# Kernel optimization log

Measured on AMD Instinct MI355X. Metric: run time of the kernel, lower is better.

The kernel has to match this reference:

```python
import jax, jax.numpy as jnp
import numpy as np

N = 100000
E = 1600000
H = 128
L = 3


def setup_inputs() -> dict:
    key = jax.random.key(0)
    ks = jax.random.split(key, 8)
    z = jax.random.normal(ks[0], (N, H), dtype=jnp.float32)
    edge_index = jax.random.randint(ks[1], (2, E), 0, N, dtype=jnp.int64)
    edge_weight = jax.random.uniform(ks[2], (E,), dtype=jnp.float32)
    s = 1.0 / np.sqrt(H)
    weight = jax.random.uniform(ks[3], (L, H, H), minval=-s, maxval=s, dtype=jnp.float32)
    w_ih = jax.random.uniform(ks[4], (3 * H, H), minval=-s, maxval=s, dtype=jnp.float32)
    w_hh = jax.random.uniform(ks[5], (3 * H, H), minval=-s, maxval=s, dtype=jnp.float32)
    b_ih = jax.random.uniform(ks[6], (3 * H,), minval=-s, maxval=s, dtype=jnp.float32)
    b_hh = jax.random.uniform(ks[7], (3 * H,), minval=-s, maxval=s, dtype=jnp.float32)
    return {"z": z, "edge_weight": edge_weight, "weight": weight,
            "w_ih": w_ih, "w_hh": w_hh, "b_ih": b_ih, "b_hh": b_hh,
            "edge_index": edge_index}


def _gru_cell(m, h, w_ih, w_hh, b_ih, b_hh):
    # torch GRUCell: gate order (r, z, n)
    gi = m @ w_ih.T + b_ih   # [N, 3H]
    gh = h @ w_hh.T + b_hh   # [N, 3H]
    i_r, i_z, i_n = jnp.split(gi, 3, axis=-1)
    h_r, h_z, h_n = jnp.split(gh, 3, axis=-1)
    r = jax.nn.sigmoid(i_r + h_r)
    zg = jax.nn.sigmoid(i_z + h_z)
    n = jnp.tanh(i_n + r * h_n)
    return (1.0 - zg) * n + zg * h


def reference(z, edge_weight, weight, w_ih, w_hh, b_ih, b_hh, edge_index):
    src = edge_index[0]  # x_j gathered from source nodes
    dst = edge_index[1]  # aggregated at target nodes
    x = z  # in_channels == out_channels, so no zero padding needed
    for l in range(L):
        m = x @ weight[l]                                  # [N, H]
        msg = m[src] * edge_weight[:, None]                # [E, H]
        agg = jax.ops.segment_sum(msg, dst, num_segments=N)  # aggr='add'
        x = _gru_cell(agg, x, w_ih, w_hh, b_ih, b_hh)
    return x
```

## Files before the change

kernel.cpp:

```cpp
#include <hip/hip_runtime.h>

typedef __bf16 bf16x8 __attribute__((ext_vector_type(8)));
typedef float floatx4 __attribute__((ext_vector_type(4)));

#define NPB 256
#define NPB_SHIFT 8
#define MAXNB 1024
#define TILE 4096

static __device__ __forceinline__ float bfu_to_f(unsigned short u) {
    unsigned int x = ((unsigned int)u) << 16;
    return __builtin_bit_cast(float, x);
}
static __device__ __forceinline__ unsigned short f_to_bfu(float f) {
    unsigned int u = __builtin_bit_cast(unsigned int, f);
    unsigned int r = (u + 0x7fffu + ((u >> 16) & 1u)) >> 16;
    return (unsigned short)r;
}

__global__ void detect_k(const unsigned short* __restrict__ bih_u,
                         const unsigned int* __restrict__ ei_u,
                         int* __restrict__ flags) {
    __shared__ int sv, sz;
    int t = threadIdx.x;
    if (t == 0) { sv = 0; sz = 0; }
    __syncthreads();
    unsigned short u = bih_u[2 * t];
    unsigned int ex = (u >> 7) & 0xFF;
    if (ex >= 64 && ex < 124) atomicAdd(&sv, 1);
    if (ei_u[2 * t + 1] == 0u) atomicAdd(&sz, 1);
    __syncthreads();
    if (t == 0) {
        flags[0] = (sv >= 48) ? 1 : 0;
        flags[1] = (sz == 64) ? 1 : 0;
    }
}


__global__ void cvt_bf16_k(const void* __restrict__ in, unsigned short* __restrict__ out,
                           int n, const int* __restrict__ flags) {
    int i = blockIdx.x * 256 + threadIdx.x;
    if (i >= n) return;
    if (flags[0]) out[i] = ((const unsigned short*)in)[i];
    else out[i] = f_to_bfu(((const float*)in)[i]);
}

__global__ void cvt_bias_k(const void* __restrict__ bih, const void* __restrict__ bhh,
                           float* __restrict__ bih_f, float* __restrict__ bhh_f,
                           const int* __restrict__ flags) {
    int i = blockIdx.x * 256 + threadIdx.x;
    if (i >= 768) return;
    const void* src = (i < 384) ? bih : bhh;
    int j = (i < 384) ? i : i - 384;
    float v = flags[0] ? bfu_to_f(((const unsigned short*)src)[j]) : ((const float*)src)[j];
    if (i < 384) bih_f[j] = v;
    else bhh_f[j] = v;
}

__global__ void out_k(const unsigned short* __restrict__ xb, void* __restrict__ out,
                      int n, const int* __restrict__ flags) {
    int i = blockIdx.x * 256 + threadIdx.x;
    if (i >= n) return;
    if (flags[0]) ((unsigned short*)out)[i] = xb[i];
    else ((float*)out)[i] = bfu_to_f(xb[i]);
}


static __device__ __forceinline__ int load_idx(const unsigned int* eiu, size_t pos, int is64) {
    return (int)eiu[is64 ? 2 * pos : pos];
}

__global__ __launch_bounds__(256) void count_k(const unsigned int* __restrict__ eiu,
                                               int* __restrict__ bucketCnt, int E,
                                               const int* __restrict__ flags) {
    __shared__ int cnt[MAXNB];
    int t = threadIdx.x;
    for (int b = t; b < MAXNB; b += 256) cnt[b] = 0;
    __syncthreads();
    int is64 = flags[1];
    int e0 = blockIdx.x * TILE;
    int e1 = min(e0 + TILE, E);
    for (int e = e0 + t; e < e1; e += 256) {
        int d = load_idx(eiu, (size_t)E + e, is64);
        atomicAdd(&cnt[d >> NPB_SHIFT], 1);
    }
    __syncthreads();
    for (int b = t; b < MAXNB; b += 256) {
        int c = cnt[b];
        if (c) atomicAdd(&bucketCnt[b], c);
    }
}

__global__ void scanB_k(const int* __restrict__ bucketCnt, int* __restrict__ bucketBase,
                        int* __restrict__ bucketCursor, int NB, int E) {
    __shared__ int sh[MAXNB];
    int t = threadIdx.x;
    int v = (t < NB) ? bucketCnt[t] : 0;
    sh[t] = v;
    __syncthreads();
    for (int off = 1; off < MAXNB; off <<= 1) {
        int u = (t >= off) ? sh[t - off] : 0;
        __syncthreads();
        sh[t] += u;
        __syncthreads();
    }
    if (t < NB) {
        int b = sh[t] - v;
        bucketBase[t] = b;
        bucketCursor[t] = b;
    }
    if (t == 0) bucketBase[NB] = E;
}

__global__ __launch_bounds__(256) void bin_k(const unsigned int* __restrict__ eiu,
                                             const void* __restrict__ ew,
                                             int* __restrict__ bucketCursor,
                                             uint2* __restrict__ rec8, int E,
                                             const int* __restrict__ flags) {
    __shared__ int cnt[MAXNB];
    __shared__ int basel[MAXNB];
    int t = threadIdx.x;
    for (int b = t; b < MAXNB; b += 256) cnt[b] = 0;
    __syncthreads();
    int is64 = flags[1];
    int isb = flags[0];
    int e0 = blockIdx.x * TILE;
    int e1 = min(e0 + TILE, E);
    for (int e = e0 + t; e < e1; e += 256) {
        int d = load_idx(eiu, (size_t)E + e, is64);
        atomicAdd(&cnt[d >> NPB_SHIFT], 1);
    }
    __syncthreads();
    for (int b = t; b < MAXNB; b += 256) {
        int c = cnt[b];
        basel[b] = c ? atomicAdd(&bucketCursor[b], c) : 0;
        cnt[b] = 0;
    }
    __syncthreads();
    for (int e = e0 + t; e < e1; e += 256) {
        int s = load_idx(eiu, (size_t)e, is64);
        int d = load_idx(eiu, (size_t)E + e, is64);
        float w = isb ? bfu_to_f(((const unsigned short*)ew)[e]) : ((const float*)ew)[e];
        int b = d >> NPB_SHIFT;
        int p = basel[b] + atomicAdd(&cnt[b], 1);
        rec8[p] = make_uint2((unsigned int)s | ((unsigned int)(d & 255) << 20),
                             __builtin_bit_cast(unsigned int, w));
    }
}

__global__ __launch_bounds__(256) void csr_k(const uint2* __restrict__ rec8,
                                             const int* __restrict__ bucketBase,
                                             int* __restrict__ offsets,
                                             uint2* __restrict__ rec, int N, int E) {
    __shared__ int cnt[NPB];
    __shared__ int sh[NPB];
    __shared__ int cur[NPB];
    int t = threadIdx.x;
    int b = blockIdx.x;
    int n0 = b << NPB_SHIFT;
    int nodes = min(NPB, N - n0);
    int ebase = bucketBase[b];
    int ecnt = bucketBase[b + 1] - ebase;

    cnt[t] = 0;
    __syncthreads();
    for (int i = t; i < ecnt; i += 256) {
        int d = (rec8[ebase + i].x >> 20) & 255;
        atomicAdd(&cnt[d], 1);
    }
    __syncthreads();
    int v = cnt[t];
    sh[t] = v;
    __syncthreads();
    for (int off = 1; off < NPB; off <<= 1) {
        int u = (t >= off) ? sh[t - off] : 0;
        __syncthreads();
        sh[t] += u;
        __syncthreads();
    }
    int loff = sh[t] - v;
    if (t < nodes) offsets[n0 + t] = ebase + loff;
    cur[t] = ebase + loff;
    if (b == 0 && t == 0) offsets[N] = E;
    __syncthreads();
    for (int i = t; i < ecnt; i += 256) {
        uint2 r = rec8[ebase + i];
        int d = (r.x >> 20) & 255;
        int p = atomicAdd(&cur[d], 1);
        rec[p] = make_uint2(r.x & 0xFFFFFu, r.y);
    }
}


static __device__ __forceinline__ float dot8_bf(uint4 wv, uint4 iv) {
    float s;
    s  = bfu_to_f((unsigned short)(wv.x)) * bfu_to_f((unsigned short)(iv.x));
    s += bfu_to_f((unsigned short)(wv.x >> 16)) * bfu_to_f((unsigned short)(iv.x >> 16));
    s += bfu_to_f((unsigned short)(wv.y)) * bfu_to_f((unsigned short)(iv.y));
    s += bfu_to_f((unsigned short)(wv.y >> 16)) * bfu_to_f((unsigned short)(iv.y >> 16));
    s += bfu_to_f((unsigned short)(wv.z)) * bfu_to_f((unsigned short)(iv.z));
    s += bfu_to_f((unsigned short)(wv.z >> 16)) * bfu_to_f((unsigned short)(iv.z >> 16));
    s += bfu_to_f((unsigned short)(wv.w)) * bfu_to_f((unsigned short)(iv.w));
    s += bfu_to_f((unsigned short)(wv.w >> 16)) * bfu_to_f((unsigned short)(iv.w >> 16));
    return s;
}

__global__ void make_ut_k(const void* __restrict__ weight, const void* __restrict__ wih,
                          unsigned short* __restrict__ Ut, const int* __restrict__ flags) {
    int idx = blockIdx.x * 256 + threadIdx.x;
    if (idx >= 3 * 384 * 128) return;
    int isb = flags[0];
    int a = idx & 127;
    int j = (idx >> 7) % 384;
    int l = idx / (384 * 128);
    float s = 0.f;
    if (isb) {
        const uint4* W4 = (const uint4*)((const unsigned short*)weight + (size_t)l * 16384 + a * 128);
        const uint4* I4 = (const uint4*)((const unsigned short*)wih + (size_t)j * 128);
#pragma unroll
        for (int c = 0; c < 16; c++) s += dot8_bf(W4[c], I4[c]);
    } else {
        const float4* W4 = (const float4*)((const float*)weight + (size_t)l * 16384 + a * 128);
        const float4* I4 = (const float4*)((const float*)wih + (size_t)j * 128);
#pragma unroll
        for (int c = 0; c < 32; c++) {
            float4 w = W4[c], i = I4[c];
            s += w.x * i.x + w.y * i.y + w.z * i.z + w.w * i.w;
        }
    }
    Ut[idx] = f_to_bfu(s);
}

__global__ void pack_b_k(const unsigned short* __restrict__ Ut,
                         const void* __restrict__ whh,
                         unsigned short* __restrict__ Bp,
                         const int* __restrict__ flags) {
    int idx = blockIdx.x * 256 + threadIdx.x;
    if (idx >= 3 * 4 * 12 * 4 * 64) return;
    int lane = idx & 63;
    int kc = (idx >> 6) & 3;
    int rest = idx >> 8;
    int j = rest % 12;
    int cg = (rest / 12) & 3;
    int l = rest / 48;
    int s = j / 6;
    int g = (j % 6) >> 1;
    int t = j & 1;
    int col = (cg * 2 + t) * 16 + (lane & 15);
    int k = kc * 32 + (lane >> 4) * 8;
    int row384 = g * 128 + col;
    unsigned short tmp[8];
    const unsigned short* src;
    if (s == 0) {
        src = Ut + (size_t)l * 49152 + row384 * 128 + k;
    } else if (flags[0]) {
        src = (const unsigned short*)whh + (size_t)row384 * 128 + k;
    } else {
        const float* wf = (const float*)whh + (size_t)row384 * 128 + k;
        for (int i = 0; i < 8; i++) tmp[i] = f_to_bfu(wf[i]);
        src = tmp;
    }
    unsigned short* dst = Bp + (size_t)l * 98304 + (((size_t)(cg * 12 + j) * 4 + kc) * 64 + lane) * 8;
    for (int i = 0; i < 8; i++) dst[i] = src[i];
}


__global__ __launch_bounds__(256) void agg_k(const unsigned short* __restrict__ xb,
                                             const int* __restrict__ offs,
                                             const uint2* __restrict__ rec,
                                             unsigned short* __restrict__ y, int N,
                                             int nch) {
    int bid = blockIdx.x;
    int c = ((bid & 7) << 3) + ((bid >> 3) & 7) + ((bid >> 6) << 6);
    if (c >= nch) return;
    int node = c * 16 + (threadIdx.x >> 4);
    int l16 = threadIdx.x & 15;
    if (node >= N) return;
    int b = offs[node];
    int e2 = offs[node + 1];
    const uint4* xp4 = (const uint4*)xb;
    float a0[8], a1[8];
#pragma unroll
    for (int i = 0; i < 8; i++) { a0[i] = 0.f; a1[i] = 0.f; }

    auto fma_row = [&](float* acc, uint4 v, float w) {
        acc[0] += w * __builtin_bit_cast(float, v.x << 16);
        acc[1] += w * __builtin_bit_cast(float, v.x & 0xffff0000u);
        acc[2] += w * __builtin_bit_cast(float, v.y << 16);
        acc[3] += w * __builtin_bit_cast(float, v.y & 0xffff0000u);
        acc[4] += w * __builtin_bit_cast(float, v.z << 16);
        acc[5] += w * __builtin_bit_cast(float, v.z & 0xffff0000u);
        acc[6] += w * __builtin_bit_cast(float, v.w << 16);
        acc[7] += w * __builtin_bit_cast(float, v.w & 0xffff0000u);
    };

    int e = b;
    for (; e + 4 <= e2; e += 4) {
        uint2 r0 = rec[e], r1 = rec[e + 1], r2 = rec[e + 2], r3 = rec[e + 3];
        uint4 v0 = xp4[(size_t)r0.x * 16 + l16];
        uint4 v1 = xp4[(size_t)r1.x * 16 + l16];
        uint4 v2 = xp4[(size_t)r2.x * 16 + l16];
        uint4 v3 = xp4[(size_t)r3.x * 16 + l16];
        fma_row(a0, v0, __builtin_bit_cast(float, r0.y));
        fma_row(a1, v1, __builtin_bit_cast(float, r1.y));
        fma_row(a0, v2, __builtin_bit_cast(float, r2.y));
        fma_row(a1, v3, __builtin_bit_cast(float, r3.y));
    }
    for (; e < e2; e++) {
        uint2 r = rec[e];
        uint4 v = xp4[(size_t)r.x * 16 + l16];
        fma_row(a0, v, __builtin_bit_cast(float, r.y));
    }

    uint4 o;
    o.x = (unsigned int)f_to_bfu(a0[0] + a1[0]) | ((unsigned int)f_to_bfu(a0[1] + a1[1]) << 16);
    o.y = (unsigned int)f_to_bfu(a0[2] + a1[2]) | ((unsigned int)f_to_bfu(a0[3] + a1[3]) << 16);
    o.z = (unsigned int)f_to_bfu(a0[4] + a1[4]) | ((unsigned int)f_to_bfu(a0[5] + a1[5]) << 16);
    o.w = (unsigned int)f_to_bfu(a0[6] + a1[6]) | ((unsigned int)f_to_bfu(a0[7] + a1[7]) << 16);
    ((uint4*)y)[(size_t)node * 16 + l16] = o;
}


__global__ __launch_bounds__(512, 4) void gru_k(const unsigned short* __restrict__ y,
                                                const unsigned short* __restrict__ xin,
                                                unsigned short* __restrict__ xout,
                                                const unsigned short* __restrict__ Bp,
                                                const float* __restrict__ bih,
                                                const float* __restrict__ bhh, int N) {
    __shared__ uint4 Blds[3072];

    int bid = blockIdx.x;
    int r8 = bid & 7;
    int inner = bid >> 3;
    int cg = inner & 3;
    int rb = ((inner >> 2) << 3) + r8;
    int row0 = rb << 7;
    if (row0 >= N) return;

    int tid = threadIdx.x;
    {
        const uint4* bsrc = (const uint4*)(Bp + (size_t)cg * 24576);
#pragma unroll
        for (int i = 0; i < 6; i++) Blds[tid + i * 512] = bsrc[tid + i * 512];
    }
    __syncthreads();

    int wave = tid >> 6;
    int wc = wave & 1;
    int wr = wave >> 1;
    int lane = tid & 63;
    int quad = lane >> 4;
    int m16 = lane & 15;
    const unsigned short* bl = (const unsigned short*)Blds;

    int rA[2];
#pragma unroll
    for (int rt = 0; rt < 2; rt++) {
        int r = row0 + wr * 32 + rt * 16 + m16;
        rA[rt] = (r < N) ? r : N - 1;
    }

    floatx4 acc[2][4];
#pragma unroll
    for (int rt = 0; rt < 2; rt++)
#pragma unroll
        for (int s = 0; s < 4; s++) acc[rt][s] = (floatx4){0.f, 0.f, 0.f, 0.f};

    bf16x8 aY[2][4], aX[2][4];

#pragma unroll
    for (int rt = 0; rt < 2; rt++)
#pragma unroll
        for (int kc = 0; kc < 4; kc++)
            aY[rt][kc] = *(const bf16x8*)(y + (size_t)rA[rt] * 128 + kc * 32 + quad * 8);
    __builtin_amdgcn_sched_barrier(0);

#pragma unroll
    for (int rt = 0; rt < 2; rt++)
#pragma unroll
        for (int kc = 0; kc < 4; kc++)
            aX[rt][kc] = *(const bf16x8*)(xin + (size_t)rA[rt] * 128 + kc * 32 + quad * 8);

#pragma unroll
    for (int kc = 0; kc < 4; kc++) {
#pragma unroll
        for (int g = 0; g < 3; g++) {
            int jU = g * 2 + wc;
            bf16x8 b = *(const bf16x8*)(bl + ((size_t)(jU * 4 + kc) * 64 + lane) * 8);
            int s = (g == 2) ? 2 : g;
            acc[0][s] = __builtin_amdgcn_mfma_f32_16x16x32_bf16(aY[0][kc], b, acc[0][s], 0, 0, 0);
            acc[1][s] = __builtin_amdgcn_mfma_f32_16x16x32_bf16(aY[1][kc], b, acc[1][s], 0, 0, 0);
        }
    }
    __builtin_amdgcn_sched_barrier(0);

#pragma unroll
    for (int kc = 0; kc < 4; kc++) {
#pragma unroll
        for (int g = 0; g < 3; g++) {
            int jW = 6 + g * 2 + wc;
            bf16x8 b = *(const bf16x8*)(bl + ((size_t)(jW * 4 + kc) * 64 + lane) * 8);
            int s = (g == 2) ? 3 : g;
            acc[0][s] = __builtin_amdgcn_mfma_f32_16x16x32_bf16(aX[0][kc], b, acc[0][s], 0, 0, 0);
            acc[1][s] = __builtin_amdgcn_mfma_f32_16x16x32_bf16(aX[1][kc], b, acc[1][s], 0, 0, 0);
        }
    }

    int ch = cg * 32 + wc * 16 + m16;
    float b_r = bih[ch] + bhh[ch];
    float b_z = bih[128 + ch] + bhh[128 + ch];
    float bi_n = bih[256 + ch];
    float bh_n = bhh[256 + ch];
#pragma unroll
    for (int rt = 0; rt < 2; rt++) {
#pragma unroll
        for (int ri = 0; ri < 4; ri++) {
            int row = row0 + wr * 32 + rt * 16 + quad * 4 + ri;
            if (row >= N) continue;
            float sr = acc[rt][0][ri] + b_r;
            float sz = acc[rt][1][ri] + b_z;
            float gn = acc[rt][2][ri] + bi_n;
            float hn = acc[rt][3][ri] + bh_n;
            float r = __builtin_amdgcn_rcpf(1.f + __expf(-sr));
            float zg = __builtin_amdgcn_rcpf(1.f + __expf(-sz));
            float x2 = gn + r * hn;
            float n = 1.f - 2.f * __builtin_amdgcn_rcpf(1.f + __expf(2.f * x2));
            float h = bfu_to_f(xin[(size_t)row * 128 + ch]);
            float o = n + zg * (h - n);
            xout[(size_t)row * 128 + ch] = f_to_bfu(o);
        }
    }
}


extern "C" void kernel_launch(void* const* d_in, const int* in_sizes, int n_in,
                              void* d_out, int out_size, void* d_ws, size_t ws_size,
                              hipStream_t stream) {
    const int N = in_sizes[0] / 128;
    const int E = in_sizes[1];
    const int NB = (N + NPB - 1) >> NPB_SHIFT;

    const void* z = d_in[0];
    const void* ew = d_in[1];
    const void* weight = d_in[2];
    const void* wih = d_in[3];
    const void* whh = d_in[4];
    const void* bih = d_in[5];
    const void* bhh = d_in[6];
    const unsigned int* eiu = (const unsigned int*)d_in[7];

    unsigned short* y = (unsigned short*)d_out;

    size_t off = 0;
    char* base = (char*)d_ws;
    auto carve = [&](size_t bytes) -> void* {
        void* p = base + off;
        off = (off + bytes + 255) & ~(size_t)255;
        return p;
    };
    unsigned short* xb = (unsigned short*)carve((size_t)N * 128 * 2);
    unsigned short* xb2 = (unsigned short*)carve((size_t)N * 128 * 2);
    uint2* rec8 = (uint2*)carve((size_t)E * 8);
    uint2* rec = (uint2*)carve((size_t)E * 8);
    int* offsets = (int*)carve((size_t)(N + 1) * 4);
    int* bucketCnt = (int*)carve(MAXNB * 4);
    int* bucketBase = (int*)carve((MAXNB + 1) * 4);
    int* bucketCursor = (int*)carve(MAXNB * 4);
    unsigned short* Ut = (unsigned short*)carve((size_t)3 * 384 * 128 * 2);
    unsigned short* Bp = (unsigned short*)carve((size_t)3 * 48 * 4 * 64 * 8 * 2);
    float* bih_f = (float*)carve(384 * 4);
    float* bhh_f = (float*)carve(384 * 4);
    int* flags = (int*)carve(256);

    detect_k<<<1, 64, 0, stream>>>((const unsigned short*)bih, eiu, flags);

    cvt_bf16_k<<<(N * 128 + 255) / 256, 256, 0, stream>>>(z, xb, N * 128, flags);
    cvt_bias_k<<<3, 256, 0, stream>>>(bih, bhh, bih_f, bhh_f, flags);

    hipMemsetAsync(bucketCnt, 0, MAXNB * 4, stream);
    int gbin = (E + TILE - 1) / TILE;
    count_k<<<gbin, 256, 0, stream>>>(eiu, bucketCnt, E, flags);
    scanB_k<<<1, MAXNB, 0, stream>>>(bucketCnt, bucketBase, bucketCursor, NB, E);
    bin_k<<<gbin, 256, 0, stream>>>(eiu, ew, bucketCursor, rec8, E, flags);
    csr_k<<<NB, NPB, 0, stream>>>(rec8, bucketBase, offsets, rec, N, E);

    make_ut_k<<<(3 * 384 * 128 + 255) / 256, 256, 0, stream>>>(weight, wih, Ut, flags);
    pack_b_k<<<(3 * 4 * 12 * 4 * 64 + 255) / 256, 256, 0, stream>>>(Ut, whh, Bp, flags);

    const int RB = (N + 127) >> 7;
    const int grid_gru = 8 * ((RB + 7) >> 3) * 4;
    const int nch = (N + 15) >> 4;
    const int grid_agg = ((nch + 63) >> 6) << 6;

    const unsigned short* cur = xb;
    unsigned short* nxt = xb2;
    for (int l = 0; l < 3; l++) {
        agg_k<<<grid_agg, 256, 0, stream>>>(cur, offsets, rec, y, N, nch);
        gru_k<<<grid_gru, 512, 0, stream>>>(y, cur, nxt, Bp + (size_t)l * 98304,
                                            bih_f, bhh_f, N);
        const unsigned short* tmp = cur;
        cur = nxt;
        nxt = (unsigned short*)tmp;
    }

    out_k<<<(N * 128 + 255) / 256, 256, 0, stream>>>(cur, d_out, N * 128, flags);
}
```

Before: 607.4 us.

## Fuse neighbor aggregation into GRU kernel via LDS-staged aggregated rows

Merges the gather-aggregate kernel and the GRU MFMA kernel into one kernel per layer. Each block aggregates its 128 rows into a swizzled LDS buffer, then loops over the four output column groups, prefetching the next weight slice into registers. This removes the global write and re-read of the aggregated activations and one launch per layer. In exchange it lowers block count and occupancy for the latency-bound gather, and serialises the column groups with extra barriers.

```diff
diff --git a/kernel.cpp b/kernel.cpp
--- a/kernel.cpp
+++ b/kernel.cpp
@@ -265,84 +265,78 @@
 }
 
 
-__global__ __launch_bounds__(256) void agg_k(const unsigned short* __restrict__ xb,
-                                             const int* __restrict__ offs,
-                                             const uint2* __restrict__ rec,
-                                             unsigned short* __restrict__ y, int N,
-                                             int nch) {
-    int bid = blockIdx.x;
-    int c = ((bid & 7) << 3) + ((bid >> 3) & 7) + ((bid >> 6) << 6);
-    if (c >= nch) return;
-    int node = c * 16 + (threadIdx.x >> 4);
-    int l16 = threadIdx.x & 15;
-    if (node >= N) return;
-    int b = offs[node];
-    int e2 = offs[node + 1];
-    const uint4* xp4 = (const uint4*)xb;
-    float a0[8], a1[8];
-#pragma unroll
-    for (int i = 0; i < 8; i++) { a0[i] = 0.f; a1[i] = 0.f; }
-
-    auto fma_row = [&](float* acc, uint4 v, float w) {
-        acc[0] += w * __builtin_bit_cast(float, v.x << 16);
-        acc[1] += w * __builtin_bit_cast(float, v.x & 0xffff0000u);
-        acc[2] += w * __builtin_bit_cast(float, v.y << 16);
-        acc[3] += w * __builtin_bit_cast(float, v.y & 0xffff0000u);
-        acc[4] += w * __builtin_bit_cast(float, v.z << 16);
-        acc[5] += w * __builtin_bit_cast(float, v.z & 0xffff0000u);
-        acc[6] += w * __builtin_bit_cast(float, v.w << 16);
-        acc[7] += w * __builtin_bit_cast(float, v.w & 0xffff0000u);
-    };
-
-    int e = b;
-    for (; e + 4 <= e2; e += 4) {
-        uint2 r0 = rec[e], r1 = rec[e + 1], r2 = rec[e + 2], r3 = rec[e + 3];
-        uint4 v0 = xp4[(size_t)r0.x * 16 + l16];
-        uint4 v1 = xp4[(size_t)r1.x * 16 + l16];
-        uint4 v2 = xp4[(size_t)r2.x * 16 + l16];
-        uint4 v3 = xp4[(size_t)r3.x * 16 + l16];
-        fma_row(a0, v0, __builtin_bit_cast(float, r0.y));
-        fma_row(a1, v1, __builtin_bit_cast(float, r1.y));
-        fma_row(a0, v2, __builtin_bit_cast(float, r2.y));
-        fma_row(a1, v3, __builtin_bit_cast(float, r3.y));
-    }
-    for (; e < e2; e++) {
-        uint2 r = rec[e];
-        uint4 v = xp4[(size_t)r.x * 16 + l16];
-        fma_row(a0, v, __builtin_bit_cast(float, r.y));
-    }
-
-    uint4 o;
-    o.x = (unsigned int)f_to_bfu(a0[0] + a1[0]) | ((unsigned int)f_to_bfu(a0[1] + a1[1]) << 16);
-    o.y = (unsigned int)f_to_bfu(a0[2] + a1[2]) | ((unsigned int)f_to_bfu(a0[3] + a1[3]) << 16);
-    o.z = (unsigned int)f_to_bfu(a0[4] + a1[4]) | ((unsigned int)f_to_bfu(a0[5] + a1[5]) << 16);
-    o.w = (unsigned int)f_to_bfu(a0[6] + a1[6]) | ((unsigned int)f_to_bfu(a0[7] + a1[7]) << 16);
-    ((uint4*)y)[(size_t)node * 16 + l16] = o;
-}
-
-
-__global__ __launch_bounds__(512, 4) void gru_k(const unsigned short* __restrict__ y,
-                                                const unsigned short* __restrict__ xin,
-                                                unsigned short* __restrict__ xout,
-                                                const unsigned short* __restrict__ Bp,
-                                                const float* __restrict__ bih,
-                                                const float* __restrict__ bhh, int N) {
+__global__ __launch_bounds__(512, 4) void fused_k(const unsigned short* __restrict__ xin,
+                                                  unsigned short* __restrict__ xout,
+                                                  const int* __restrict__ offs,
+                                                  const uint2* __restrict__ rec,
+                                                  const unsigned short* __restrict__ Bp,
+                                                  const float* __restrict__ bih,
+                                                  const float* __restrict__ bhh, int N) {
+    __shared__ unsigned short Ylds[16384];
     __shared__ uint4 Blds[3072];
 
-    int bid = blockIdx.x;
-    int r8 = bid & 7;
-    int inner = bid >> 3;
-    int cg = inner & 3;
-    int rb = ((inner >> 2) << 3) + r8;
-    int row0 = rb << 7;
-    if (row0 >= N) return;
-
     int tid = threadIdx.x;
+    int row0 = blockIdx.x << 7;
+
+    uint4 breg[6];
     {
-        const uint4* bsrc = (const uint4*)(Bp + (size_t)cg * 24576);
-#pragma unroll
-        for (int i = 0; i < 6; i++) Blds[tid + i * 512] = bsrc[tid + i * 512];
-    }
+        const uint4* bsrc = (const uint4*)Bp;
+#pragma unroll
+        for (int i = 0; i < 6; i++) breg[i] = bsrc[tid + i * 512];
+    }
+
+    {
+        const uint4* xp4 = (const uint4*)xin;
+        int l16 = tid & 15;
+        int rr = tid >> 4;
+        auto fma_row = [&](float* acc, uint4 v, float w) {
+            acc[0] += w * __builtin_bit_cast(float, v.x << 16);
+            acc[1] += w * __builtin_bit_cast(float, v.x & 0xffff0000u);
+            acc[2] += w * __builtin_bit_cast(float, v.y << 16);
+            acc[3] += w * __builtin_bit_cast(float, v.y & 0xffff0000u);
+            acc[4] += w * __builtin_bit_cast(float, v.z << 16);
+            acc[5] += w * __builtin_bit_cast(float, v.z & 0xffff0000u);
+            acc[6] += w * __builtin_bit_cast(float, v.w << 16);
+            acc[7] += w * __builtin_bit_cast(float, v.w & 0xffff0000u);
+        };
+        for (int gi = 0; gi < 4; gi++) {
+            int r = gi * 32 + rr;
+            int node = row0 + r;
+            float a0[8], a1[8];
+#pragma unroll
+            for (int i = 0; i < 8; i++) { a0[i] = 0.f; a1[i] = 0.f; }
+            if (node < N) {
+                int e = offs[node];
+                int e2 = offs[node + 1];
+                for (; e + 4 <= e2; e += 4) {
+                    uint2 r0 = rec[e], r1 = rec[e + 1], r2 = rec[e + 2], r3 = rec[e + 3];
+                    uint4 v0 = xp4[(size_t)r0.x * 16 + l16];
+                    uint4 v1 = xp4[(size_t)r1.x * 16 + l16];
+                    uint4 v2 = xp4[(size_t)r2.x * 16 + l16];
+                    uint4 v3 = xp4[(size_t)r3.x * 16 + l16];
+                    fma_row(a0, v0, __builtin_bit_cast(float, r0.y));
+                    fma_row(a1, v1, __builtin_bit_cast(float, r1.y));
+                    fma_row(a0, v2, __builtin_bit_cast(float, r2.y));
+                    fma_row(a1, v3, __builtin_bit_cast(float, r3.y));
+                }
+                for (; e < e2; e++) {
+                    uint2 rr2 = rec[e];
+                    uint4 v = xp4[(size_t)rr2.x * 16 + l16];
+                    fma_row(a0, v, __builtin_bit_cast(float, rr2.y));
+                }
+            }
+            uint4 o;
+            o.x = (unsigned int)f_to_bfu(a0[0] + a1[0]) | ((unsigned int)f_to_bfu(a0[1] + a1[1]) << 16);
+            o.y = (unsigned int)f_to_bfu(a0[2] + a1[2]) | ((unsigned int)f_to_bfu(a0[3] + a1[3]) << 16);
+            o.z = (unsigned int)f_to_bfu(a0[4] + a1[4]) | ((unsigned int)f_to_bfu(a0[5] + a1[5]) << 16);
+            o.w = (unsigned int)f_to_bfu(a0[6] + a1[6]) | ((unsigned int)f_to_bfu(a0[7] + a1[7]) << 16);
+            int u = l16 ^ (r & 15);
+            *(uint4*)&Ylds[(size_t)r * 128 + u * 8] = o;
+        }
+    }
+
+#pragma unroll
+    for (int i = 0; i < 6; i++) Blds[tid + i * 512] = breg[i];
     __syncthreads();
 
     int wave = tid >> 6;
@@ -353,81 +347,90 @@
     int m16 = lane & 15;
     const unsigned short* bl = (const unsigned short*)Blds;
 
-    int rA[2];
+    int rloc[2], rA[2];
 #pragma unroll
     for (int rt = 0; rt < 2; rt++) {
-        int r = row0 + wr * 32 + rt * 16 + m16;
-        rA[rt] = (r < N) ? r : N - 1;
-    }
-
-    floatx4 acc[2][4];
-#pragma unroll
-    for (int rt = 0; rt < 2; rt++)
-#pragma unroll
-        for (int s = 0; s < 4; s++) acc[rt][s] = (floatx4){0.f, 0.f, 0.f, 0.f};
-
-    bf16x8 aY[2][4], aX[2][4];
-
-#pragma unroll
-    for (int rt = 0; rt < 2; rt++)
-#pragma unroll
-        for (int kc = 0; kc < 4; kc++)
-            aY[rt][kc] = *(const bf16x8*)(y + (size_t)rA[rt] * 128 + kc * 32 + quad * 8);
-    __builtin_amdgcn_sched_barrier(0);
-
-#pragma unroll
-    for (int rt = 0; rt < 2; rt++)
-#pragma unroll
-        for (int kc = 0; kc < 4; kc++)
-            aX[rt][kc] = *(const bf16x8*)(xin + (size_t)rA[rt] * 128 + kc * 32 + quad * 8);
-
-#pragma unroll
-    for (int kc = 0; kc < 4; kc++) {
-#pragma unroll
-        for (int g = 0; g < 3; g++) {
-            int jU = g * 2 + wc;
-            bf16x8 b = *(const bf16x8*)(bl + ((size_t)(jU * 4 + kc) * 64 + lane) * 8);
-            int s = (g == 2) ? 2 : g;
-            acc[0][s] = __builtin_amdgcn_mfma_f32_16x16x32_bf16(aY[0][kc], b, acc[0][s], 0, 0, 0);
-            acc[1][s] = __builtin_amdgcn_mfma_f32_16x16x32_bf16(aY[1][kc], b, acc[1][s], 0, 0, 0);
-        }
-    }
-    __builtin_amdgcn_sched_barrier(0);
-
-#pragma unroll
-    for (int kc = 0; kc < 4; kc++) {
-#pragma unroll
-        for (int g = 0; g < 3; g++) {
-            int jW = 6 + g * 2 + wc;
-            bf16x8 b = *(const bf16x8*)(bl + ((size_t)(jW * 4 + kc) * 64 + lane) * 8);
-            int s = (g == 2) ? 3 : g;
-            acc[0][s] = __builtin_amdgcn_mfma_f32_16x16x32_bf16(aX[0][kc], b, acc[0][s], 0, 0, 0);
-            acc[1][s] = __builtin_amdgcn_mfma_f32_16x16x32_bf16(aX[1][kc], b, acc[1][s], 0, 0, 0);
-        }
-    }
-
-    int ch = cg * 32 + wc * 16 + m16;
-    float b_r = bih[ch] + bhh[ch];
-    float b_z = bih[128 + ch] + bhh[128 + ch];
-    float bi_n = bih[256 + ch];
-    float bh_n = bhh[256 + ch];
-#pragma unroll
-    for (int rt = 0; rt < 2; rt++) {
-#pragma unroll
-        for (int ri = 0; ri < 4; ri++) {
-            int row = row0 + wr * 32 + rt * 16 + quad * 4 + ri;
-            if (row >= N) continue;
-            float sr = acc[rt][0][ri] + b_r;
-            float sz = acc[rt][1][ri] + b_z;
-            float gn = acc[rt][2][ri] + bi_n;
-            float hn = acc[rt][3][ri] + bh_n;
-            float r = __builtin_amdgcn_rcpf(1.f + __expf(-sr));
-            float zg = __builtin_amdgcn_rcpf(1.f + __expf(-sz));
-            float x2 = gn + r * hn;
-            float n = 1.f - 2.f * __builtin_amdgcn_rcpf(1.f + __expf(2.f * x2));
-            float h = bfu_to_f(xin[(size_t)row * 128 + ch]);
-            float o = n + zg * (h - n);
-            xout[(size_t)row * 128 + ch] = f_to_bfu(o);
+        rloc[rt] = wr * 32 + rt * 16 + m16;
+        int rg = row0 + rloc[rt];
+        rA[rt] = (rg < N) ? rg : N - 1;
+    }
+
+    for (int cg = 0; cg < 4; cg++) {
+        if (cg < 3) {
+            const uint4* bsrc = (const uint4*)(Bp + (size_t)(cg + 1) * 24576);
+#pragma unroll
+            for (int i = 0; i < 6; i++) breg[i] = bsrc[tid + i * 512];
+        }
+
+        floatx4 acc[2][4];
+#pragma unroll
+        for (int rt = 0; rt < 2; rt++)
+#pragma unroll
+            for (int s = 0; s < 4; s++) acc[rt][s] = (floatx4){0.f, 0.f, 0.f, 0.f};
+
+        bf16x8 aY[2][4], aX[2][4];
+#pragma unroll
+        for (int rt = 0; rt < 2; rt++)
+#pragma unroll
+            for (int kc = 0; kc < 4; kc++) {
+                int u = (kc * 4 + quad) ^ m16;
+                aY[rt][kc] = *(const bf16x8*)&Ylds[(size_t)rloc[rt] * 128 + u * 8];
+                aX[rt][kc] = *(const bf16x8*)(xin + (size_t)rA[rt] * 128 + kc * 32 + quad * 8);
+            }
+
+#pragma unroll
+        for (int kc = 0; kc < 4; kc++) {
+#pragma unroll
+            for (int g = 0; g < 3; g++) {
+                int jU = g * 2 + wc;
+                bf16x8 b = *(const bf16x8*)(bl + ((size_t)(jU * 4 + kc) * 64 + lane) * 8);
+                int s = (g == 2) ? 2 : g;
+                acc[0][s] = __builtin_amdgcn_mfma_f32_16x16x32_bf16(aY[0][kc], b, acc[0][s], 0, 0, 0);
+                acc[1][s] = __builtin_amdgcn_mfma_f32_16x16x32_bf16(aY[1][kc], b, acc[1][s], 0, 0, 0);
+            }
+        }
+#pragma unroll
+        for (int kc = 0; kc < 4; kc++) {
+#pragma unroll
+            for (int g = 0; g < 3; g++) {
+                int jW = 6 + g * 2 + wc;
+                bf16x8 b = *(const bf16x8*)(bl + ((size_t)(jW * 4 + kc) * 64 + lane) * 8);
+                int s = (g == 2) ? 3 : g;
+                acc[0][s] = __builtin_amdgcn_mfma_f32_16x16x32_bf16(aX[0][kc], b, acc[0][s], 0, 0, 0);
+                acc[1][s] = __builtin_amdgcn_mfma_f32_16x16x32_bf16(aX[1][kc], b, acc[1][s], 0, 0, 0);
+            }
+        }
+
+        int ch = cg * 32 + wc * 16 + m16;
+        float b_r = bih[ch] + bhh[ch];
+        float b_z = bih[128 + ch] + bhh[128 + ch];
+        float bi_n = bih[256 + ch];
+        float bh_n = bhh[256 + ch];
+#pragma unroll
+        for (int rt = 0; rt < 2; rt++) {
+#pragma unroll
+            for (int ri = 0; ri < 4; ri++) {
+                int row = row0 + wr * 32 + rt * 16 + quad * 4 + ri;
+                if (row >= N) continue;
+                float sr = acc[rt][0][ri] + b_r;
+                float sz = acc[rt][1][ri] + b_z;
+                float gn = acc[rt][2][ri] + bi_n;
+                float hn = acc[rt][3][ri] + bh_n;
+                float r = __builtin_amdgcn_rcpf(1.f + __expf(-sr));
+                float zg = __builtin_amdgcn_rcpf(1.f + __expf(-sz));
+                float x2 = gn + r * hn;
+                float n = 1.f - 2.f * __builtin_amdgcn_rcpf(1.f + __expf(2.f * x2));
+                float h = bfu_to_f(xin[(size_t)row * 128 + ch]);
+                float o = n + zg * (h - n);
+                xout[(size_t)row * 128 + ch] = f_to_bfu(o);
+            }
+        }
+
+        __syncthreads();
+        if (cg < 3) {
+#pragma unroll
+            for (int i = 0; i < 6; i++) Blds[tid + i * 512] = breg[i];
+            __syncthreads();
         }
     }
 }
@@ -448,8 +451,6 @@
     const void* bih = d_in[5];
     const void* bhh = d_in[6];
     const unsigned int* eiu = (const unsigned int*)d_in[7];
-
-    unsigned short* y = (unsigned short*)d_out;
 
     size_t off = 0;
     char* base = (char*)d_ws;
@@ -488,16 +489,12 @@
     pack_b_k<<<(3 * 4 * 12 * 4 * 64 + 255) / 256, 256, 0, stream>>>(Ut, whh, Bp, flags);
 
     const int RB = (N + 127) >> 7;
-    const int grid_gru = 8 * ((RB + 7) >> 3) * 4;
-    const int nch = (N + 15) >> 4;
-    const int grid_agg = ((nch + 63) >> 6) << 6;
 
     const unsigned short* cur = xb;
     unsigned short* nxt = xb2;
     for (int l = 0; l < 3; l++) {
-        agg_k<<<grid_agg, 256, 0, stream>>>(cur, offsets, rec, y, N, nch);
-        gru_k<<<grid_gru, 512, 0, stream>>>(y, cur, nxt, Bp + (size_t)l * 98304,
-                                            bih_f, bhh_f, N);
+        fused_k<<<RB, 512, 0, stream>>>(cur, nxt, offsets, rec, Bp + (size_t)l * 98304,
+                                        bih_f, bhh_f, N);
         const unsigned short* tmp = cur;
         cur = nxt;
         nxt = (unsigned short*)tmp;
```

Measured after the change: 766.1 us. 26.1% more time.
